# Performance work log

Measured on AMD Instinct MI355X. Metric: run time of the kernel, lower is better.

The kernel has to match this reference:

```python
import jax, jax.numpy as jnp
import numpy as np
from jax import lax

DN = ('NCHW', 'OIHW', 'NCHW')

def _conv(x, w, b):
    # Conv2d(k=4, stride=2, padding=1): H -> H/2
    y = lax.conv_general_dilated(x, w, (2, 2), ((1, 1), (1, 1)), dimension_numbers=DN)
    return y + b[None, :, None, None]

def _deconv(x, w, b):
    # ConvTranspose2d(k=4, stride=2, padding=1): H -> 2H.
    # Equivalent dense conv: flip kernel spatially, swap in/out channels,
    # lhs_dilation = stride, padding = k-1-p = 2.
    wf = jnp.flip(w, (2, 3)).transpose(1, 0, 2, 3)  # (out, in, 4, 4)
    y = lax.conv_general_dilated(x, wf, (1, 1), ((2, 2), (2, 2)), lhs_dilation=(2, 2), dimension_numbers=DN)
    return y + b[None, :, None, None]

def setup_inputs() -> dict:
    key = jax.random.key(0)
    ks = jax.random.split(key, 20)
    f = jnp.float32
    s = 0.05  # small init scale for stability
    inp = {
        'x':   jax.random.uniform(ks[0], (64, 3, 224, 224), dtype=f),
        # encoder conv weights (OIHW) + biases
        'ew1': jax.random.normal(ks[1], (32, 3, 4, 4), f) * s,   'eb1': jnp.zeros((32,), f),
        'ew2': jax.random.normal(ks[2], (64, 32, 4, 4), f) * s,  'eb2': jnp.zeros((64,), f),
        'ew3': jax.random.normal(ks[3], (128, 64, 4, 4), f) * s, 'eb3': jnp.zeros((128,), f),
        'ew4': jax.random.normal(ks[4], (64, 128, 4, 4), f) * s, 'eb4': jnp.zeros((64,), f),
        # codebook: uniform(-1/K, 1/K) like torch init, K=4000, D=12544
        'emb': jax.random.uniform(ks[5], (4000, 12544), f, -1.0 / 4000, 1.0 / 4000),
        # decoder conv-transpose weights in torch layout (in, out, kh, kw) + biases
        'dw1': jax.random.normal(ks[6], (64, 128, 4, 4), f) * s, 'db1': jnp.zeros((128,), f),
        'dw2': jax.random.normal(ks[7], (128, 64, 4, 4), f) * s, 'db2': jnp.zeros((64,), f),
        'dw3': jax.random.normal(ks[8], (64, 32, 4, 4), f) * s,  'db3': jnp.zeros((32,), f),
        'dw4': jax.random.normal(ks[9], (32, 3, 4, 4), f) * s,   'db4': jnp.zeros((3,), f),
    }
    return inp

def reference(x, ew1, eb1, ew2, eb2, ew3, eb3, ew4, eb4, emb,
              dw1, db1, dw2, db2, dw3, db3, dw4, db4):
    sg = lax.stop_gradient
    B = x.shape[0]
    # ---- Encoder ----
    h = jax.nn.relu(_conv(x, ew1, eb1))
    h = jax.nn.relu(_conv(h, ew2, eb2))
    h = jax.nn.relu(_conv(h, ew3, eb3))
    h = _conv(h, ew4, eb4)                 # (B, 64, 14, 14)
    z = h.reshape(B, -1)                   # (B, 12544)
    # ---- Vector quantization ----
    # ||z||^2 - 2 z E^T + ||e||^2, argmin over codebook
    dist = (jnp.sum(z * z, axis=1, keepdims=True)
            - 2.0 * (z @ emb.T)
            + jnp.sum(emb * emb, axis=1))  # (B, 4000)
    idx = jnp.argmin(dist, axis=1)         # (B,)
    quantized = emb[idx]                   # (B, 12544) -- direct gather (== onehot @ emb)
    e_latent = jnp.mean((sg(quantized) - z) ** 2)
    q_latent = jnp.mean((quantized - sg(z)) ** 2)
    vq_loss = q_latent + 0.25 * e_latent
    zq = z + sg(quantized - z)             # straight-through
    # ---- Decoder ----
    d = zq.reshape(B, 64, 14, 14)
    d = jax.nn.relu(_deconv(d, dw1, db1))
    d = jax.nn.relu(_deconv(d, dw2, db2))
    d = jax.nn.relu(_deconv(d, dw3, db3))
    x_recon = jax.nn.sigmoid(_deconv(d, dw4, db4))  # (B, 3, 224, 224)
    recon_loss = jnp.mean((x_recon - x) ** 2)
    loss = recon_loss + vq_loss
    return (x_recon, loss, recon_loss, vq_loss)
```

## Files before the change

### kernel.cpp

```cpp
#include <hip/hip_runtime.h>
#include <math.h>

typedef unsigned short u16;
typedef unsigned int u32;
typedef __attribute__((ext_vector_type(8))) short short8;
typedef __attribute__((ext_vector_type(4))) float f32x4;

__device__ __forceinline__ u16 f2bf(float f) {
    u32 u = __float_as_uint(f);
    u = u + 0x7fffu + ((u >> 16) & 1u);
    return (u16)(u >> 16);
}
__device__ __forceinline__ float bf2f(u16 h) { return __uint_as_float(((u32)h) << 16); }

__device__ __forceinline__ f32x4 mfma16(short8 a, short8 b, f32x4 c) {
    return __builtin_amdgcn_mfma_f32_16x16x32_bf16(a, b, c, 0, 0, 0);
}

__device__ __forceinline__ uint4 pack8(float4 a, float4 b) {
    uint4 r;
    r.x = (u32)f2bf(a.x) | ((u32)f2bf(a.y) << 16);
    r.y = (u32)f2bf(a.z) | ((u32)f2bf(a.w) << 16);
    r.z = (u32)f2bf(b.x) | ((u32)f2bf(b.y) << 16);
    r.w = (u32)f2bf(b.z) | ((u32)f2bf(b.w) << 16);
    return r;
}

#define GLOAD_LDS16(gsrc, ldst)                                                      \
    __builtin_amdgcn_global_load_lds(                                                \
        (__attribute__((address_space(1))) u32*)(gsrc),                              \
        (__attribute__((address_space(3))) u32*)(ldst), 16, 0, 0)

__device__ __forceinline__ void prep1_item(const float* __restrict__ w,
                                           u16* __restrict__ o, int i)
{
    int j = i & 7; int kx = j >> 1, cp = j & 1;
    int r = i >> 3;
    int co = r & 31; int r2 = r >> 5;
    int ky = r2 & 3; int h = r2 >> 2;
    int ci = 2 * h + cp;
    o[i] = (ci < 3) ? f2bf(w[((co * 3 + ci) * 16) + ky * 4 + kx]) : (u16)0;
}
__device__ __forceinline__ void prepc_item(const float* __restrict__ w,
                                           u16* __restrict__ o, int CIN, int COUT, int i)
{
    int j = i & 7; int r = i >> 3;
    int co = r % COUT; int r2 = r / COUT;
    int tap = r2 & 15; int ch = r2 >> 4;
    int ci = ch * 8 + j;
    o[i] = f2bf(w[((size_t)co * CIN + ci) * 16 + tap]);
}
__device__ __forceinline__ void prepd_item(const float* __restrict__ w,
                                           u16* __restrict__ o, int CIN, int COUT,
                                           int COPAD, int i)
{
    int j = i & 7; int r = i >> 3;
    int co = r % COPAD; int r2 = r / COPAD;
    int t16 = r2 & 15; int ch = r2 >> 4;
    int py = t16 >> 3, px = (t16 >> 2) & 1, qq = t16 & 3;
    int ta = qq >> 1, tb = qq & 1;
    int ky = py + 2 * ta, kx = px + 2 * tb;
    int ci = ch * 8 + j;
    o[i] = (co < COUT) ? f2bf(w[(((size_t)ci * COUT + co) * 16) + ky * 4 + kx]) : (u16)0;
}

__global__ __launch_bounds__(256) void prep_all(
    const float* __restrict__ ew1, const float* __restrict__ ew2,
    const float* __restrict__ ew3, const float* __restrict__ ew4,
    const float* __restrict__ dw1, const float* __restrict__ dw2,
    const float* __restrict__ dw3, const float* __restrict__ dw4,
    u16* __restrict__ w1c, u16* __restrict__ wc2,
    u16* __restrict__ wc3, u16* __restrict__ wc4,
    u16* __restrict__ wd1, u16* __restrict__ wd2,
    u16* __restrict__ wd3, u16* __restrict__ wd4)
{
    int i = blockIdx.x * 256 + threadIdx.x;
    if (i < 2048) { prep1_item(ew1, w1c, i); return; }
    i -= 2048;
    if (i < 32768)  { prepc_item(ew2, wc2, 32, 64, i); return; }
    i -= 32768;
    if (i < 131072) { prepc_item(ew3, wc3, 64, 128, i); return; }
    i -= 131072;
    if (i < 131072) { prepc_item(ew4, wc4, 128, 64, i); return; }
    i -= 131072;
    if (i < 131072) { prepd_item(dw1, wd1, 64, 128, 128, i); return; }
    i -= 131072;
    if (i < 131072) { prepd_item(dw2, wd2, 128, 64, 64, i); return; }
    i -= 131072;
    if (i < 32768)  { prepd_item(dw3, wd3, 64, 32, 32, i); return; }
    i -= 32768;
    if (i < 8192)   { prepd_item(dw4, wd4, 32, 3, 16, i); return; }
}

template<int CIN, int COUT, int COTILE, int H2, int W2, int NSEG, int MB,
         int MBW, int NWF, int RELU, int STOREZ>
__global__ __launch_bounds__(256) void conv_mfma(
    const u16* __restrict__ in, const u16* __restrict__ wcvt,
    const float* __restrict__ bias, u16* __restrict__ outp,
    float* __restrict__ z32)
{
    constexpr int CHUNKS = CIN / 8, CGI = CIN / 8, CGO = COUT / 8;
    constexpr int HIN = H2 * 2, WIN = W2 * 2, SLOTW = 35;
    constexpr int NF = COTILE / 16, WM = MB / MBW, WN = NF / NWF;
    static_assert(WM * WN == 4, "wave layout");
    constexpr int TBu = MB * 4 * SLOTW, WBu = 16 * COTILE;
    constexpr int EBu = (MB * 16 * COTILE * 2 + 15) / 16;
    constexpr int SM = (TBu + WBu) > EBu ? (TBu + WBu) : EBu;
    __shared__ uint4 smem[SM];
    uint4* T = smem; uint4* wS = smem + TBu;
    u16* E = (u16*)smem;

    const int tid = threadIdx.x, wid = tid >> 6, lane = tid & 63;
    const int q = lane >> 4, lm = lane & 15;
    const int wm = wid / WN, wn = wid % WN;
    const int cobase = blockIdx.y * COTILE;
    const int mbase = blockIdx.x * MB;

    f32x4 acc[MBW][NWF];
    #pragma unroll
    for (int a = 0; a < MBW; ++a)
        #pragma unroll
        for (int b = 0; b < NWF; ++b) {
            acc[a][b][0] = 0.f; acc[a][b][1] = 0.f;
            acc[a][b][2] = 0.f; acc[a][b][3] = 0.f;
        }

    for (int ch = 0; ch < CHUNKS; ++ch) {
        __syncthreads();
        for (int ib = 0; ib < TBu; ib += 256) {
            int i = ib + tid;
            uint4* ldst = T + ib + (wid << 6);
            if (i < TBu) {
                int mb = i / (4 * SLOTW), r2 = i % (4 * SLOTW);
                int r = r2 / SLOTW, s = r2 % SLOTW;
                int mbg = mbase + mb;
                int n = mbg / (H2 * NSEG), rr = mbg % (H2 * NSEG);
                int oy = rr / NSEG, ox0 = (rr % NSEG) << 4;
                int iy = 2 * oy - 1 + r, ix = 2 * ox0 - 1 + s;
                if ((unsigned)iy < (unsigned)HIN && (unsigned)ix < (unsigned)WIN) {
                    GLOAD_LDS16(in + (size_t)(((n * CGI + ch) * HIN + iy) * WIN + ix) * 8, ldst);
                } else {
                    uint4 zz = {0u, 0u, 0u, 0u};
                    T[i] = zz;
                }
            }
        }
        for (int ib = 0; ib < WBu; ib += 256) {
            int i = ib + tid;
            int tap = i / COTILE, co = i % COTILE;
            GLOAD_LDS16(wcvt + (size_t)((ch * 16 + tap) * COUT + cobase + co) * 8,
                        wS + ib + (wid << 6));
        }
        __syncthreads();
        #pragma unroll
        for (int ky = 0; ky < 4; ++ky) {
            short8 Af[MBW]; short8 Bf[NWF];
            #pragma unroll
            for (int im = 0; im < MBW; ++im) {
                int mb = wm * MBW + im;
                Af[im] = *(const short8*)(T + (mb * 4 + ky) * SLOTW + 2 * lm + q);
            }
            #pragma unroll
            for (int inf = 0; inf < NWF; ++inf)
                Bf[inf] = *(const short8*)(wS + (ky * 4 + q) * COTILE + wn * NWF * 16 + inf * 16 + lm);
            #pragma unroll
            for (int im = 0; im < MBW; ++im)
                #pragma unroll
                for (int inf = 0; inf < NWF; ++inf)
                    acc[im][inf] = mfma16(Af[im], Bf[inf], acc[im][inf]);
        }
    }
    __syncthreads();
    #pragma unroll
    for (int inf = 0; inf < NWF; ++inf) {
        int col = wn * NWF * 16 + inf * 16 + lm;
        float bv = bias[cobase + col];
        #pragma unroll
        for (int im = 0; im < MBW; ++im) {
            int pixb = (wm * MBW + im) * 16 + q * 4;
            #pragma unroll
            for (int r = 0; r < 4; ++r) {
                float v = acc[im][inf][r] + bv;
                if (RELU) v = fmaxf(v, 0.f);
                E[(pixb + r) * COTILE + col] = f2bf(v);
            }
        }
    }
    __syncthreads();
    for (int i = tid; i < MB * 16 * (COTILE / 8); i += 256) {
        int pix = i / (COTILE / 8), cg = i % (COTILE / 8);
        int mb = pix >> 4, m = pix & 15;
        int mbg = mbase + mb;
        int n = mbg / (H2 * NSEG), rr = mbg % (H2 * NSEG);
        int oy = rr / NSEG, ox0 = (rr % NSEG) << 4;
        int ox = ox0 + m;
        if (ox < W2)
            *(uint4*)(outp + (size_t)(((n * CGO + cobase / 8 + cg) * H2 + oy) * W2 + ox) * 8) =
                *(uint4*)(E + pix * COTILE + cg * 8);
    }
    if (STOREZ) {
        for (int i = tid; i < MB * 16 * COTILE; i += 256) {
            int pix = i / COTILE, co = i % COTILE;
            int mb = pix >> 4, m = pix & 15;
            int mbg = mbase + mb;
            int n = mbg / (H2 * NSEG), rr = mbg % (H2 * NSEG);
            int oy = rr / NSEG, ox0 = (rr % NSEG) << 4;
            int ox = ox0 + m;
            if (ox < W2)
                z32[(size_t)((n * COUT + cobase + co) * H2 + oy) * W2 + ox] =
                    bf2f(E[pix * COTILE + co]);
        }
    }
}

__global__ __launch_bounds__(256) void conv1_mfma(
    const float* __restrict__ x, const u16* __restrict__ w1c,
    const float* __restrict__ bias, u16* __restrict__ outp)
{
    constexpr int MB = 16, MBW = 4, NWF = 2, COTILE = 32, W2 = 112, H2 = 112, NSEG = 7;
    constexpr int TBu = MB * 2 * 64, WBu = 256;
    __shared__ uint4 smem[TBu + WBu];
    uint4* T1 = smem; uint4* w1S = smem + TBu;
    u16* E = (u16*)smem;

    const int tid = threadIdx.x, wid = tid >> 6, lane = tid & 63;
    const int q = lane >> 4, lm = lane & 15;
    const int wm = wid;
    const int mbase = blockIdx.x * MB;

    f32x4 acc[MBW][NWF];
    #pragma unroll
    for (int a = 0; a < MBW; ++a)
        #pragma unroll
        for (int b = 0; b < NWF; ++b) {
            acc[a][b][0] = 0.f; acc[a][b][1] = 0.f;
            acc[a][b][2] = 0.f; acc[a][b][3] = 0.f;
        }

    for (int i = tid; i < TBu; i += 256) {
        int mb = i >> 7; int r = i & 127;
        int h = r >> 6; int r2 = r & 63;
        int ky = r2 >> 4; int m = r2 & 15;
        int mbg = mbase + mb;
        int n = mbg / (H2 * NSEG), rr = mbg % (H2 * NSEG);
        int oy = rr / NSEG, ox0 = (rr % NSEG) << 4;
        int iy = 2 * oy - 1 + ky;
        int ixb = 2 * (ox0 + m) - 1;
        u32 u[4];
        #pragma unroll
        for (int kx = 0; kx < 4; ++kx) {
            float v0 = 0.f, v1 = 0.f;
            int ix = ixb + kx;
            if ((unsigned)iy < 224u && (unsigned)ix < 224u) {
                int ci0 = 2 * h;
                v0 = x[((size_t)(n * 3 + ci0) * 224 + iy) * 224 + ix];
                if (ci0 + 1 < 3) v1 = x[((size_t)(n * 3 + ci0 + 1) * 224 + iy) * 224 + ix];
            }
            u[kx] = (u32)f2bf(v0) | ((u32)f2bf(v1) << 16);
        }
        uint4 vv; vv.x = u[0]; vv.y = u[1]; vv.z = u[2]; vv.w = u[3];
        T1[i] = vv;
    }
    if (tid < 256) {
        w1S[tid] = *(const uint4*)(w1c + (size_t)tid * 8);
    }
    __syncthreads();
    #pragma unroll
    for (int h = 0; h < 2; ++h) {
        short8 Af[MBW]; short8 Bf[NWF];
        #pragma unroll
        for (int im = 0; im < MBW; ++im) {
            int mb = wm * MBW + im;
            Af[im] = *(const short8*)(T1 + (mb * 2 + h) * 64 + lane);
        }
        #pragma unroll
        for (int inf = 0; inf < NWF; ++inf)
            Bf[inf] = *(const short8*)(w1S + (h * 4 + q) * 32 + inf * 16 + lm);
        #pragma unroll
        for (int im = 0; im < MBW; ++im)
            #pragma unroll
            for (int inf = 0; inf < NWF; ++inf)
                acc[im][inf] = mfma16(Af[im], Bf[inf], acc[im][inf]);
    }
    __syncthreads();
    #pragma unroll
    for (int inf = 0; inf < NWF; ++inf) {
        int col = inf * 16 + lm;
        float bv = bias[col];
        #pragma unroll
        for (int im = 0; im < MBW; ++im) {
            int pixb = (wm * MBW + im) * 16 + q * 4;
            #pragma unroll
            for (int r = 0; r < 4; ++r) {
                float v = fmaxf(acc[im][inf][r] + bv, 0.f);
                E[(pixb + r) * COTILE + col] = f2bf(v);
            }
        }
    }
    __syncthreads();
    for (int i = tid; i < MB * 16 * (COTILE / 8); i += 256) {
        int pix = i / (COTILE / 8), cg = i % (COTILE / 8);
        int mb = pix >> 4, m = pix & 15;
        int mbg = mbase + mb;
        int n = mbg / (H2 * NSEG), rr = mbg % (H2 * NSEG);
        int oy = rr / NSEG, ox0 = (rr % NSEG) << 4;
        int ox = ox0 + m;
        *(uint4*)(outp + (size_t)(((n * 4 + cg) * H2 + oy) * W2 + ox) * 8) =
            *(uint4*)(E + pix * COTILE + cg * 8);
    }
}

template<int CIN, int COUT, int COPAD, int COTILE, int Hp, int Wp, int NSEG,
         int MB, int MBW, int NWF, int RELU>
__global__ __launch_bounds__(256) void deconv_mfma(
    const u16* __restrict__ in, const u16* __restrict__ dcvt,
    const float* __restrict__ bias, u16* __restrict__ outp)
{
    constexpr int CHUNKS = CIN / 8, CGI = CIN / 8, CGO = COUT / 8;
    constexpr int SLOTW = 17;
    constexpr int NF = COTILE / 16, WM = MB / MBW, WN = NF / NWF;
    static_assert(WM * WN == 4, "wave layout");
    constexpr int BPP = 64 * Hp * NSEG / MB;
    constexpr int TBu = MB * 2 * SLOTW, WBu = 4 * COTILE;
    constexpr int EBu = (MB * 16 * COTILE * 2 + 15) / 16;
    constexpr int SM = (TBu + WBu) > EBu ? (TBu + WBu) : EBu;
    __shared__ uint4 smem[SM];
    uint4* T = smem; uint4* wS = smem + TBu;
    u16* E = (u16*)smem;

    const int tid = threadIdx.x, wid = tid >> 6, lane = tid & 63;
    const int q = lane >> 4, lm = lane & 15;
    const int wm = wid / WN, wn = wid % WN;
    const int par = blockIdx.x / BPP;
    const int py = par >> 1, px = par & 1;
    const int mbase = (blockIdx.x % BPP) * MB;
    const int cobase = blockIdx.y * COTILE;

    f32x4 acc[MBW][NWF];
    #pragma unroll
    for (int a = 0; a < MBW; ++a)
        #pragma unroll
        for (int b = 0; b < NWF; ++b) {
            acc[a][b][0] = 0.f; acc[a][b][1] = 0.f;
            acc[a][b][2] = 0.f; acc[a][b][3] = 0.f;
        }

    for (int ch = 0; ch < CHUNKS; ++ch) {
        __syncthreads();
        for (int ib = 0; ib < TBu; ib += 256) {
            int i = ib + tid;
            uint4* ldst = T + ib + (wid << 6);
            if (i < TBu) {
                int mb = i / (2 * SLOTW), r2 = i % (2 * SLOTW);
                int rr_ = r2 / SLOTW, s = r2 % SLOTW;
                int mbg = mbase + mb;
                int n = mbg / (Hp * NSEG), rm = mbg % (Hp * NSEG);
                int oyp = rm / NSEG, u0 = (rm % NSEG) << 4;
                int iy = oyp + (1 - py) - 1 + rr_;
                int ix = u0 + (1 - px) - 1 + s;
                if ((unsigned)iy < (unsigned)Hp && (unsigned)ix < (unsigned)Wp) {
                    GLOAD_LDS16(in + (size_t)(((n * CGI + ch) * Hp + iy) * Wp + ix) * 8, ldst);
                } else {
                    uint4 zz = {0u, 0u, 0u, 0u};
                    T[i] = zz;
                }
            }
        }
        for (int ib = 0; ib < WBu; ib += 256) {
            int i = ib + tid;
            if (i < WBu) {
                int qq = i / COTILE, co = i % COTILE;
                GLOAD_LDS16(dcvt + (size_t)((ch * 16 + par * 4 + qq) * COPAD + cobase + co) * 8,
                            wS + ib + (wid << 6));
            }
        }
        __syncthreads();
        {
            short8 Af[MBW]; short8 Bf[NWF];
            #pragma unroll
            for (int im = 0; im < MBW; ++im) {
                int mb = wm * MBW + im;
                Af[im] = *(const short8*)(T + (mb * 2 + (1 - (q >> 1))) * SLOTW + lm + 1 - (q & 1));
            }
            #pragma unroll
            for (int inf = 0; inf < NWF; ++inf)
                Bf[inf] = *(const short8*)(wS + q * COTILE + wn * NWF * 16 + inf * 16 + lm);
            #pragma unroll
            for (int im = 0; im < MBW; ++im)
                #pragma unroll
                for (int inf = 0; inf < NWF; ++inf)
                    acc[im][inf] = mfma16(Af[im], Bf[inf], acc[im][inf]);
        }
    }
    __syncthreads();
    #pragma unroll
    for (int inf = 0; inf < NWF; ++inf) {
        int col = wn * NWF * 16 + inf * 16 + lm;
        float bv = bias[cobase + col];
        #pragma unroll
        for (int im = 0; im < MBW; ++im) {
            int pixb = (wm * MBW + im) * 16 + q * 4;
            #pragma unroll
            for (int r = 0; r < 4; ++r) {
                float v = acc[im][inf][r] + bv;
                if (RELU) v = fmaxf(v, 0.f);
                E[(pixb + r) * COTILE + col] = f2bf(v);
            }
        }
    }
    __syncthreads();
    for (int i = tid; i < MB * 16 * (COTILE / 8); i += 256) {
        int pix = i / (COTILE / 8), cg = i % (COTILE / 8);
        int mb = pix >> 4, m = pix & 15;
        int mbg = mbase + mb;
        int n = mbg / (Hp * NSEG), rm = mbg % (Hp * NSEG);
        int oyp = rm / NSEG, u0 = (rm % NSEG) << 4;
        int u = u0 + m;
        if (u < Wp) {
            int ox = 2 * u + (px ? 0 : 1);
            int oy = 2 * oyp + (py ? 0 : 1);
            *(uint4*)(outp + (size_t)(((n * CGO + cobase / 8 + cg) * (2 * Hp) + oy) * (2 * Wp) + ox) * 8) =
                *(uint4*)(E + pix * COTILE + cg * 8);
        }
    }
}

__global__ __launch_bounds__(256) void deconv4_mfma(
    const u16* __restrict__ in, const u16* __restrict__ dcvt,
    const float* __restrict__ bias, float* __restrict__ outp,
    const float* __restrict__ xref, float* __restrict__ bpart)
{
    constexpr int Hp = 112, Wp = 112, NSEG = 7, MB = 16, MBW = 4;
    constexpr int CGI = 4, CHUNKS = 4;
    constexpr int TROW = 3, TCOL = 18;
    constexpr int TBu = MB * TROW * TCOL;
    __shared__ uint4 smem[TBu + 1024];
    __shared__ float red[4];
    uint4* T = smem; uint4* wS = smem + TBu;
    float* Ef = (float*)smem;

    const int tid = threadIdx.x, wid = tid >> 6, lane = tid & 63;
    const int q = lane >> 4, lm = lane & 15;
    const int wm = wid;
    const int mbase = blockIdx.x * MB;

    f32x4 acc[4][MBW];
    #pragma unroll
    for (int p = 0; p < 4; ++p)
        #pragma unroll
        for (int a = 0; a < MBW; ++a) {
            acc[p][a][0] = 0.f; acc[p][a][1] = 0.f; acc[p][a][2] = 0.f; acc[p][a][3] = 0.f;
        }

    for (int ib = 0; ib < 1024; ib += 256)
        GLOAD_LDS16(dcvt + (size_t)(ib + tid) * 8, wS + ib + (wid << 6));

    for (int ch = 0; ch < CHUNKS; ++ch) {
        __syncthreads();
        for (int ib = 0; ib < TBu; ib += 256) {
            int i = ib + tid;
            uint4* ldst = T + ib + (wid << 6);
            if (i < TBu) {
                int mb = i / (TROW * TCOL), r2 = i % (TROW * TCOL);
                int r = r2 / TCOL, s = r2 % TCOL;
                int mbg = mbase + mb;
                int n = mbg / (Hp * NSEG), rm = mbg % (Hp * NSEG);
                int oyp = rm / NSEG, u0 = (rm % NSEG) << 4;
                int iy = oyp - 1 + r;
                int ix = u0 - 1 + s;
                if ((unsigned)iy < (unsigned)Hp && (unsigned)ix < (unsigned)Wp) {
                    GLOAD_LDS16(in + (size_t)(((n * CGI + ch) * Hp + iy) * Wp + ix) * 8, ldst);
                } else {
                    uint4 zz = {0u, 0u, 0u, 0u};
                    T[i] = zz;
                }
            }
        }
        __syncthreads();
        #pragma unroll
        for (int par = 0; par < 4; ++par) {
            const int py = par >> 1, px = par & 1;
            short8 Bf = *(const short8*)(wS + (ch * 16 + par * 4 + q) * 16 + lm);
            #pragma unroll
            for (int im = 0; im < MBW; ++im) {
                int mb = wm * MBW + im;
                short8 Af = *(const short8*)(T + (mb * TROW + (2 - py - (q >> 1))) * TCOL
                                             + lm + 2 - px - (q & 1));
                acc[par][im] = mfma16(Af, Bf, acc[par][im]);
            }
        }
    }

    __syncthreads();
    if (lm < 3) {
        float bv = bias[lm];
        #pragma unroll
        for (int par = 0; par < 4; ++par)
            #pragma unroll
            for (int im = 0; im < MBW; ++im)
                #pragma unroll
                for (int r = 0; r < 4; ++r)
                    Ef[(((wm * MBW + im) * 16 + q * 4 + r) * 4 + par) * 3 + lm] =
                        acc[par][im][r] + bv;
    }
    __syncthreads();
    float lsum = 0.f;
    #pragma unroll
    for (int k = 0; k < 3; ++k) {
        int i = k * 256 + tid;
        int mb = i / 48, rem = i % 48;
        int row = rem / 24, rem2 = rem % 24;
        int co = rem2 / 8, ox4 = rem2 % 8;
        int mbg = mbase + mb;
        int n = mbg / (Hp * NSEG), rm = mbg % (Hp * NSEG);
        int oyp = rm / NSEG, u0 = (rm % NSEG) << 4;
        int pA = row ? 1 : 3, pB = row ? 0 : 2;
        int uL = 2 * ox4, uH = uL + 1;
        float v0 = Ef[((mb * 16 + uL) * 4 + pA) * 3 + co];
        float v1 = Ef[((mb * 16 + uL) * 4 + pB) * 3 + co];
        float v2 = Ef[((mb * 16 + uH) * 4 + pA) * 3 + co];
        float v3 = Ef[((mb * 16 + uH) * 4 + pB) * 3 + co];
        float4 sv;
        sv.x = 1.f / (1.f + expf(-v0));
        sv.y = 1.f / (1.f + expf(-v1));
        sv.z = 1.f / (1.f + expf(-v2));
        sv.w = 1.f / (1.f + expf(-v3));
        size_t ro = ((size_t)(n * 3 + co) * 224 + 2 * oyp + row) * 224 + 2 * u0 + 4 * ox4;
        float4 x4 = *(const float4*)(xref + ro);
        *(float4*)(outp + ro) = sv;
        float d0 = sv.x - x4.x, d1 = sv.y - x4.y, d2 = sv.z - x4.z, d3 = sv.w - x4.w;
        lsum += d0 * d0 + d1 * d1 + d2 * d2 + d3 * d3;
    }
    #pragma unroll
    for (int off = 32; off > 0; off >>= 1)
        lsum += __shfl_down(lsum, off, 64);
    if (lane == 0) red[wid] = lsum;
    __syncthreads();
    if (tid == 0)
        bpart[blockIdx.x] = red[0] + red[1] + red[2] + red[3];
}

__global__ __launch_bounds__(256) void vq_gemm(
    const float* __restrict__ z32, const float* __restrict__ emb,
    float* __restrict__ P, float* __restrict__ normp)
{
    __shared__ uint4 As[8 * 64];
    __shared__ uint4 Bs[8 * 256];
    const int tid = threadIdx.x, wid = tid >> 6, lane = tid & 63;
    const int q = lane >> 4, lm = lane & 15;
    const int jt = blockIdx.x, ks = blockIdx.y;
    const int jg = jt * 256 + tid;
    const int jc = jg < 4000 ? jg : 3999;
    const float* brow = emb + (size_t)jc * 12544 + ks * 896;
    const int m = tid & 63, ksub = tid >> 6;
    const float* arow = z32 + (size_t)m * 12544 + ks * 896 + ksub * 16;

    f32x4 acc[4][4];
    #pragma unroll
    for (int a = 0; a < 4; ++a)
        #pragma unroll
        for (int b = 0; b < 4; ++b) {
            acc[a][b][0] = 0.f; acc[a][b][1] = 0.f; acc[a][b][2] = 0.f; acc[a][b][3] = 0.f;
        }
    float nsq = 0.f;

    for (int ch = 0; ch < 14; ++ch) {
        __syncthreads();
        {
            float4 f0 = *(const float4*)(arow + ch * 64);
            float4 f1 = *(const float4*)(arow + ch * 64 + 4);
            float4 f2 = *(const float4*)(arow + ch * 64 + 8);
            float4 f3 = *(const float4*)(arow + ch * 64 + 12);
            As[(ksub * 2 + 0) * 64 + m] = pack8(f0, f1);
            As[(ksub * 2 + 1) * 64 + m] = pack8(f2, f3);
        }
        {
            const float* bp = brow + ch * 64;
            #pragma unroll
            for (int ko = 0; ko < 8; ++ko) {
                float4 fa = *(const float4*)(bp + ko * 8);
                float4 fb = *(const float4*)(bp + ko * 8 + 4);
                nsq += fa.x * fa.x + fa.y * fa.y + fa.z * fa.z + fa.w * fa.w
                     + fb.x * fb.x + fb.y * fb.y + fb.z * fb.z + fb.w * fb.w;
                Bs[ko * 256 + tid] = pack8(fa, fb);
            }
        }
        __syncthreads();
        #pragma unroll
        for (int kk = 0; kk < 2; ++kk) {
            short8 Af[4]; short8 Bf[4];
            #pragma unroll
            for (int mf = 0; mf < 4; ++mf)
                Af[mf] = *(const short8*)(As + (kk * 4 + q) * 64 + mf * 16 + lm);
            #pragma unroll
            for (int nf = 0; nf < 4; ++nf)
                Bf[nf] = *(const short8*)(Bs + (kk * 4 + q) * 256 + wid * 64 + nf * 16 + lm);
            #pragma unroll
            for (int mf = 0; mf < 4; ++mf)
                #pragma unroll
                for (int nf = 0; nf < 4; ++nf)
                    acc[mf][nf] = mfma16(Af[mf], Bf[nf], acc[mf][nf]);
        }
    }
    #pragma unroll
    for (int mf = 0; mf < 4; ++mf)
        #pragma unroll
        for (int nf = 0; nf < 4; ++nf) {
            int j = jt * 256 + wid * 64 + nf * 16 + lm;
            if (j < 4000) {
                #pragma unroll
                for (int r = 0; r < 4; ++r) {
                    int b = mf * 16 + q * 4 + r;
                    P[(size_t)(ks * 64 + b) * 4000 + j] = acc[mf][nf][r];
                }
            }
        }
    if (jg < 4000) normp[ks * 4000 + jg] = nsq;
}

__global__ __launch_bounds__(256) void vq_argmin_gather(
    const float* __restrict__ P, const float* __restrict__ normp,
    const float* __restrict__ emb, const float* __restrict__ z32,
    u16* __restrict__ Qb, float* __restrict__ vacc)
{
    const int b = blockIdx.x;
    const int tid = threadIdx.x;
    float best = 3.4e38f;
    int bidx = 0x7fffffff;
    for (int j = tid; j < 4000; j += 256) {
        float dot = 0.f, nrm = 0.f;
        #pragma unroll
        for (int s = 0; s < 14; ++s) {
            dot += P[(size_t)(s * 64 + b) * 4000 + j];
            nrm += normp[s * 4000 + j];
        }
        float d = nrm - 2.f * dot;
        if (d < best) { best = d; bidx = j; }
    }
    __shared__ float sv[256];
    __shared__ int si[256];
    sv[tid] = best; si[tid] = bidx;
    __syncthreads();
    for (int off = 128; off > 0; off >>= 1) {
        if (tid < off) {
            float v2 = sv[tid + off]; int i2 = si[tid + off];
            if (v2 < sv[tid] || (v2 == sv[tid] && i2 < si[tid])) { sv[tid] = v2; si[tid] = i2; }
        }
        __syncthreads();
    }
    const int code = si[0];
    const float* e = emb + (size_t)code * 12544;
    const float* zb = z32 + (size_t)b * 12544;
    float ls = 0.f;
    for (int d = tid; d < 12544; d += 256) {
        float ev = e[d];
        int co = d / 196, rem = d % 196;
        int y = rem / 14, xx = rem % 14;
        Qb[((size_t)((b * 8 + (co >> 3)) * 14 + y) * 14 + xx) * 8 + (co & 7)] = f2bf(ev);
        float df = ev - zb[d];
        ls += df * df;
    }
    #pragma unroll
    for (int off = 32; off > 0; off >>= 1)
        ls += __shfl_down(ls, off, 64);
    if ((tid & 63) == 0) atomicAdd(vacc, ls);
}

__global__ __launch_bounds__(256) void reduce_final(
    const float* __restrict__ bpart, const float* __restrict__ vacc,
    float* __restrict__ tail)
{
    const int tid = threadIdx.x;
    float s = 0.f;
    for (int i = tid; i < 3136; i += 256) s += bpart[i];
    #pragma unroll
    for (int off = 32; off > 0; off >>= 1)
        s += __shfl_down(s, off, 64);
    __shared__ float red[4];
    if ((tid & 63) == 0) red[tid >> 6] = s;
    __syncthreads();
    if (tid == 0) {
        float rsum = red[0] + red[1] + red[2] + red[3];
        float recon = rsum * (1.f / 9633792.f);
        float vq = 1.25f * vacc[0] * (1.f / 802816.f);
        tail[0] = recon + vq;
        tail[1] = recon;
        tail[2] = vq;
    }
}

extern "C" void kernel_launch(void* const* d_in, const int* in_sizes, int n_in,
                              void* d_out, int out_size, void* d_ws, size_t ws_size,
                              hipStream_t stream)
{
    const float* x   = (const float*)d_in[0];
    const float* ew1 = (const float*)d_in[1];
    const float* eb1 = (const float*)d_in[2];
    const float* ew2 = (const float*)d_in[3];
    const float* eb2 = (const float*)d_in[4];
    const float* ew3 = (const float*)d_in[5];
    const float* eb3 = (const float*)d_in[6];
    const float* ew4 = (const float*)d_in[7];
    const float* eb4 = (const float*)d_in[8];
    const float* emb = (const float*)d_in[9];
    const float* dw1 = (const float*)d_in[10];
    const float* db1 = (const float*)d_in[11];
    const float* dw2 = (const float*)d_in[12];
    const float* db2 = (const float*)d_in[13];
    const float* dw3 = (const float*)d_in[14];
    const float* db3 = (const float*)d_in[15];
    const float* dw4 = (const float*)d_in[16];
    const float* db4 = (const float*)d_in[17];
    float* out = (float*)d_out;

    size_t off = 0;
    char* base = (char*)d_ws;
    auto nxt = [&](size_t bytes) -> char* {
        char* p = base + off;
        off = (off + bytes + 255) & ~(size_t)255;
        return p;
    };
    u16*   A1    = (u16*)nxt(25690112ull * 2);
    u16*   A2    = (u16*)nxt(12845056ull * 2);
    u16*   A3    = (u16*)nxt(6422528ull * 2);
    float* z32   = (float*)nxt(802816ull * 4);
    u16*   Qb    = (u16*)nxt(802816ull * 2);
    float* P     = (float*)nxt(14ull * 64 * 4000 * 4);
    float* normp = (float*)nxt(14ull * 4000 * 4);
    u16*   w1c   = (u16*)nxt(2048ull * 2);
    u16*   wc2   = (u16*)nxt(32768ull * 2);
    u16*   wc3   = (u16*)nxt(131072ull * 2);
    u16*   wc4   = (u16*)nxt(131072ull * 2);
    u16*   wd1   = (u16*)nxt(131072ull * 2);
    u16*   wd2   = (u16*)nxt(131072ull * 2);
    u16*   wd3   = (u16*)nxt(32768ull * 2);
    u16*   wd4   = (u16*)nxt(8192ull * 2);
    float* accp  = (float*)nxt(512);
    float* bpart = (float*)nxt(3136ull * 4);
    u16*   D1 = A3;
    u16*   D2 = A2;
    u16*   D3 = A1;

    hipMemsetAsync(accp, 0, 8, stream);

    prep_all<<<2344, 256, 0, stream>>>(ew1, ew2, ew3, ew4, dw1, dw2, dw3, dw4,
                                       w1c, wc2, wc3, wc4, wd1, wd2, wd3, wd4);

    conv1_mfma<<<3136, 256, 0, stream>>>(x, w1c, eb1, A1);
    conv_mfma<32, 64, 64, 56, 56, 4, 16, 8, 2, 1, 0>
        <<<dim3(896, 1), 256, 0, stream>>>(A1, wc2, eb2, A2, nullptr);
    conv_mfma<64, 128, 64, 28, 28, 2, 8, 4, 2, 1, 0>
        <<<dim3(448, 2), 256, 0, stream>>>(A2, wc3, eb3, A3, nullptr);
    conv_mfma<128, 64, 64, 14, 14, 1, 8, 2, 4, 0, 1>
        <<<dim3(112, 1), 256, 0, stream>>>(A3, wc4, eb4, Qb, z32);

    vq_gemm<<<dim3(16, 14), 256, 0, stream>>>(z32, emb, P, normp);
    vq_argmin_gather<<<64, 256, 0, stream>>>(P, normp, emb, z32, Qb, accp);

    deconv_mfma<64, 128, 128, 64, 14, 14, 1, 8, 4, 2, 1>
        <<<dim3(448, 2), 256, 0, stream>>>(Qb, wd1, db1, D1);
    deconv_mfma<128, 64, 64, 64, 28, 28, 2, 16, 8, 2, 1>
        <<<dim3(896, 1), 256, 0, stream>>>(D1, wd2, db2, D2);
    deconv_mfma<64, 32, 32, 32, 56, 56, 4, 16, 8, 1, 1>
        <<<dim3(3584, 1), 256, 0, stream>>>(D2, wd3, db3, D3);
    deconv4_mfma<<<3136, 256, 0, stream>>>(D3, wd4, db4, out, x, bpart);

    reduce_final<<<1, 256, 0, stream>>>(bpart, accp, out + 9633792);
}
```

Measured before the change: 695.5 us.

## Coalesce VQ GEMM global loads with XOR-swizzled LDS and vectorize conv1 input loads

The VQ distance GEMM used to have each thread stream its own codebook row (stride 12544 floats between threads), so global loads were poorly coalesced. Now eight consecutive threads cover contiguous 32-byte pieces of one row, and LDS stores use an XOR swizzle to avoid bank conflicts. Per-row squared norms become partial sums that are reduced through an extra shared buffer. Separately, the first encoder conv gathers interior input pixels with float4 loads instead of scalar loads, keeping the scalar path for edges.

Result: slower. 716.7 us (+3.1%).

```diff
diff --git a/kernel.cpp b/kernel.cpp
--- a/kernel.cpp
+++ b/kernel.cpp
@@ -246,19 +246,32 @@
         int oy = rr / NSEG, ox0 = (rr % NSEG) << 4;
         int iy = 2 * oy - 1 + ky;
         int ixb = 2 * (ox0 + m) - 1;
-        u32 u[4];
-        #pragma unroll
-        for (int kx = 0; kx < 4; ++kx) {
-            float v0 = 0.f, v1 = 0.f;
-            int ix = ixb + kx;
-            if ((unsigned)iy < 224u && (unsigned)ix < 224u) {
-                int ci0 = 2 * h;
-                v0 = x[((size_t)(n * 3 + ci0) * 224 + iy) * 224 + ix];
-                if (ci0 + 1 < 3) v1 = x[((size_t)(n * 3 + ci0 + 1) * 224 + iy) * 224 + ix];
-            }
-            u[kx] = (u32)f2bf(v0) | ((u32)f2bf(v1) << 16);
-        }
-        uint4 vv; vv.x = u[0]; vv.y = u[1]; vv.z = u[2]; vv.w = u[3];
+        int ci0 = 2 * h;
+        uint4 vv;
+        const float* rowp = x + ((size_t)(n * 3 + ci0) * 224 + iy) * 224;
+        if ((unsigned)iy < 224u && ixb >= 0 && ixb <= 220) {
+            float4 a = *(const float4*)(rowp + ixb);
+            float4 bq;
+            if (h == 0) bq = *(const float4*)(rowp + 224 * 224 + ixb);
+            else { bq.x = 0.f; bq.y = 0.f; bq.z = 0.f; bq.w = 0.f; }
+            vv.x = (u32)f2bf(a.x) | ((u32)f2bf(bq.x) << 16);
+            vv.y = (u32)f2bf(a.y) | ((u32)f2bf(bq.y) << 16);
+            vv.z = (u32)f2bf(a.z) | ((u32)f2bf(bq.z) << 16);
+            vv.w = (u32)f2bf(a.w) | ((u32)f2bf(bq.w) << 16);
+        } else {
+            u32 u[4];
+            #pragma unroll
+            for (int kx = 0; kx < 4; ++kx) {
+                float v0 = 0.f, v1 = 0.f;
+                int ix = ixb + kx;
+                if ((unsigned)iy < 224u && (unsigned)ix < 224u) {
+                    v0 = rowp[ix];
+                    if (ci0 + 1 < 3) v1 = rowp[224 * 224 + ix];
+                }
+                u[kx] = (u32)f2bf(v0) | ((u32)f2bf(v1) << 16);
+            }
+            vv.x = u[0]; vv.y = u[1]; vv.z = u[2]; vv.w = u[3];
+        }
         T1[i] = vv;
     }
     if (tid < 256) {
@@ -546,14 +559,12 @@
 {
     __shared__ uint4 As[8 * 64];
     __shared__ uint4 Bs[8 * 256];
+    __shared__ float Ns[256 * 8];
     const int tid = threadIdx.x, wid = tid >> 6, lane = tid & 63;
     const int q = lane >> 4, lm = lane & 15;
     const int jt = blockIdx.x, ks = blockIdx.y;
-    const int jg = jt * 256 + tid;
-    const int jc = jg < 4000 ? jg : 3999;
-    const float* brow = emb + (size_t)jc * 12544 + ks * 896;
-    const int m = tid & 63, ksub = tid >> 6;
-    const float* arow = z32 + (size_t)m * 12544 + ks * 896 + ksub * 16;
+    const int k8s = tid & 7;
+    const int rb2 = tid >> 3;
 
     f32x4 acc[4][4];
     #pragma unroll
@@ -562,45 +573,62 @@
         for (int b = 0; b < 4; ++b) {
             acc[a][b][0] = 0.f; acc[a][b][1] = 0.f; acc[a][b][2] = 0.f; acc[a][b][3] = 0.f;
         }
-    float nsq = 0.f;
+    float nsum[8];
+    #pragma unroll
+    for (int it = 0; it < 8; ++it) nsum[it] = 0.f;
 
     for (int ch = 0; ch < 14; ++ch) {
         __syncthreads();
-        {
-            float4 f0 = *(const float4*)(arow + ch * 64);
-            float4 f1 = *(const float4*)(arow + ch * 64 + 4);
-            float4 f2 = *(const float4*)(arow + ch * 64 + 8);
-            float4 f3 = *(const float4*)(arow + ch * 64 + 12);
-            As[(ksub * 2 + 0) * 64 + m] = pack8(f0, f1);
-            As[(ksub * 2 + 1) * 64 + m] = pack8(f2, f3);
-        }
-        {
-            const float* bp = brow + ch * 64;
-            #pragma unroll
-            for (int ko = 0; ko < 8; ++ko) {
-                float4 fa = *(const float4*)(bp + ko * 8);
-                float4 fb = *(const float4*)(bp + ko * 8 + 4);
-                nsq += fa.x * fa.x + fa.y * fa.y + fa.z * fa.z + fa.w * fa.w
-                     + fb.x * fb.x + fb.y * fb.y + fb.z * fb.z + fb.w * fb.w;
-                Bs[ko * 256 + tid] = pack8(fa, fb);
-            }
+        #pragma unroll
+        for (int it = 0; it < 2; ++it) {
+            int i = tid + it * 256;
+            int k8 = i & 7, m = i >> 3;
+            const float* ap = z32 + (size_t)m * 12544 + ks * 896 + ch * 64 + k8 * 8;
+            float4 f0 = *(const float4*)(ap);
+            float4 f1 = *(const float4*)(ap + 4);
+            As[k8 * 64 + (m ^ k8)] = pack8(f0, f1);
+        }
+        #pragma unroll
+        for (int it = 0; it < 8; ++it) {
+            int r = rb2 + 32 * it;
+            int jg = jt * 256 + r;
+            int jc = jg < 4000 ? jg : 3999;
+            const float* bp = emb + (size_t)jc * 12544 + ks * 896 + ch * 64 + k8s * 8;
+            float4 fa = *(const float4*)(bp);
+            float4 fb = *(const float4*)(bp + 4);
+            nsum[it] += fa.x * fa.x + fa.y * fa.y + fa.z * fa.z + fa.w * fa.w
+                      + fb.x * fb.x + fb.y * fb.y + fb.z * fb.z + fb.w * fb.w;
+            Bs[k8s * 256 + (r ^ k8s)] = pack8(fa, fb);
         }
         __syncthreads();
         #pragma unroll
         for (int kk = 0; kk < 2; ++kk) {
             short8 Af[4]; short8 Bf[4];
+            int k8x = kk * 4 + q;
             #pragma unroll
             for (int mf = 0; mf < 4; ++mf)
-                Af[mf] = *(const short8*)(As + (kk * 4 + q) * 64 + mf * 16 + lm);
+                Af[mf] = *(const short8*)(As + k8x * 64 + ((mf * 16 + lm) ^ k8x));
             #pragma unroll
             for (int nf = 0; nf < 4; ++nf)
-                Bf[nf] = *(const short8*)(Bs + (kk * 4 + q) * 256 + wid * 64 + nf * 16 + lm);
+                Bf[nf] = *(const short8*)(Bs + k8x * 256 + ((wid * 64 + nf * 16 + lm) ^ k8x));
             #pragma unroll
             for (int mf = 0; mf < 4; ++mf)
                 #pragma unroll
                 for (int nf = 0; nf < 4; ++nf)
                     acc[mf][nf] = mfma16(Af[mf], Bf[nf], acc[mf][nf]);
         }
+    }
+    __syncthreads();
+    #pragma unroll
+    for (int it = 0; it < 8; ++it)
+        Ns[(rb2 + 32 * it) * 8 + k8s] = nsum[it];
+    __syncthreads();
+    {
+        float s = 0.f;
+        #pragma unroll
+        for (int f = 0; f < 8; ++f) s += Ns[tid * 8 + f];
+        int jg2 = jt * 256 + tid;
+        if (jg2 < 4000) normp[ks * 4000 + jg2] = s;
     }
     #pragma unroll
     for (int mf = 0; mf < 4; ++mf)
@@ -615,7 +643,6 @@
                 }
             }
         }
-    if (jg < 4000) normp[ks * 4000 + jg] = nsq;
 }
 
 __global__ __launch_bounds__(256) void vq_argmin_gather(
```
